# Kernel tuning notes

Hardware: AMD Instinct MI355X
Metric: run time of the kernel (lower is better)

## Reference

```python
import jax, jax.numpy as jnp
import numpy as np
import math

HEAD_DIM = 64
N_Q = 64
N_KV = 8
HIDDEN = 2880
SLIDING = 128
BASE = 150000.0
INIT_CTX = 4096
SCALE = 32.0
NTK_A = 1.0
NTK_B = 32.0
SEQ = 2048


def _rope_cos_sin(position_ids):
    # YaRN-scaled inverse frequencies (scaling_factor > 1 branch)
    freq = BASE ** (jnp.arange(0, HEAD_DIM, 2, dtype=jnp.float32) / HEAD_DIM)
    concentration = 0.1 * math.log(SCALE) + 1.0
    d_half = HEAD_DIM // 2
    low = d_half * math.log(INIT_CTX / (NTK_B * 2 * math.pi)) / math.log(BASE)
    high = d_half * math.log(INIT_CTX / (NTK_A * 2 * math.pi)) / math.log(BASE)
    interpolation = 1.0 / (SCALE * freq)
    extrapolation = 1.0 / freq
    ramp = (jnp.arange(d_half, dtype=jnp.float32) - low) / (high - low)
    mask = 1.0 - jnp.clip(ramp, 0.0, 1.0)
    inv_freq = interpolation * (1.0 - mask) + extrapolation * mask
    freqs = position_ids.astype(jnp.float32)[:, None] * inv_freq[None, :]  # [n, d/2]
    return jnp.cos(freqs) * concentration, jnp.sin(freqs) * concentration


def _apply_rope(x, cos, sin):
    # x: [n, h, d]; cos/sin: [n, d/2]
    cos = cos[:, None, :].astype(x.dtype)
    sin = sin[:, None, :].astype(x.dtype)
    x1, x2 = jnp.split(x, 2, axis=-1)
    return jnp.concatenate([x1 * cos - x2 * sin, x2 * cos + x1 * sin], axis=-1)


def setup_inputs() -> dict:
    key = jax.random.key(0)
    ks = jax.random.split(key, 6)
    qkv_dim = HEAD_DIM * (N_Q + 2 * N_KV)
    return {
        "hidden_states": jax.random.normal(ks[0], (SEQ, HIDDEN), dtype=jnp.float32),
        "qkv_w": jax.random.normal(ks[1], (qkv_dim, HIDDEN), dtype=jnp.float32) * 0.02,
        "qkv_b": jax.random.normal(ks[2], (qkv_dim,), dtype=jnp.float32) * 0.02,
        "o_w": jax.random.normal(ks[3], (HIDDEN, N_Q * HEAD_DIM), dtype=jnp.float32) * 0.02,
        "o_b": jax.random.normal(ks[4], (HIDDEN,), dtype=jnp.float32) * 0.02,
        "sinks": jax.random.normal(ks[5], (N_Q,), dtype=jnp.float32),
        "position_ids": jnp.arange(SEQ, dtype=jnp.int64 if jax.config.jax_enable_x64 else jnp.int32),
    }


def reference(hidden_states, qkv_w, qkv_b, o_w, o_b, sinks, position_ids):
    n = hidden_states.shape[0]
    scaling = HEAD_DIM ** (-0.5)

    # fused QKV projection + split
    qkv = hidden_states @ qkv_w.T + qkv_b  # [n, (nq+2*nkv)*d]
    q_sz, k_sz = N_Q * HEAD_DIM, N_KV * HEAD_DIM
    q = qkv[:, :q_sz].reshape(n, N_Q, HEAD_DIM)
    k = qkv[:, q_sz:q_sz + k_sz].reshape(n, N_KV, HEAD_DIM)
    v = qkv[:, q_sz + k_sz:].reshape(n, N_KV, HEAD_DIM)

    # RoPE (YaRN)
    cos, sin = _rope_cos_sin(position_ids)
    q = _apply_rope(q, cos, sin)
    k = _apply_rope(k, cos, sin)

    # GQA: repeat KV heads to match query heads
    groups = N_Q // N_KV
    k_full = jnp.repeat(k, groups, axis=1)  # [n, N_Q, d]
    v_full = jnp.repeat(v, groups, axis=1)

    scores = jnp.einsum('qhd,khd->hqk', q, k_full) * scaling  # [H, S, S]

    # sliding-window mask (distance > window -> -inf), as in source (no causal term)
    current_pos = position_ids.max()
    key_pos = current_pos - n + 1 + jnp.arange(n)
    dist = position_ids[:, None] - key_pos[None, :]
    win_mask = jnp.where(dist > SLIDING, -jnp.inf, 0.0).astype(scores.dtype)
    scores = scores + win_mask[None, :, :]

    # learned sink logit appended to softmax normalization
    sink = jnp.broadcast_to(sinks[:, None, None], (N_Q, n, 1)).astype(scores.dtype)
    logits = jnp.concatenate([scores, sink], axis=-1)  # [H, S, S+1]
    probs = jax.nn.softmax(logits, axis=-1)[..., :-1]   # drop sink column

    attn = jnp.einsum('hqk,khd->qhd', probs, v_full)    # [S, H, d]
    attn = attn.reshape(n, N_Q * HEAD_DIM)
    return attn @ o_w.T + o_b
```

## Files before the change

### kernel.cpp

```cpp
#include <hip/hip_runtime.h>
#include <hip/hip_bf16.h>
#include <stdint.h>

typedef __attribute__((ext_vector_type(4))) float f32x4;
typedef __attribute__((ext_vector_type(8))) short bf16x8;

#define SEQ 2048
#define HIDDEN 2880
#define NQ 64
#define NKV 8
#define HD 64
#define QKV_DIM 5120
#define Q_SZ 4096
#define K_SZ 512
#define OW_N 2880
#define OW_NPAD 2944
#define OW_K 4096

__device__ __forceinline__ unsigned short f2b_bits(float f) {
    unsigned int x = __float_as_uint(f);
    unsigned int r = (x + 0x7fffu + ((x >> 16) & 1u)) >> 16;
    return (unsigned short)r;
}
__device__ __forceinline__ float b2f(unsigned short u) {
    return __uint_as_float(((unsigned int)u) << 16);
}

__device__ __forceinline__ void llds16(const ushort* g, ushort* l) {
    __builtin_amdgcn_global_load_lds(
        (const __attribute__((address_space(1))) void*)g,
        (__attribute__((address_space(3))) void*)l, 16, 0, 0);
}

__global__ void convert_all(const float* __restrict__ hidden, const float* __restrict__ qkv_w,
                            const float* __restrict__ o_w, ushort* __restrict__ hs_bf,
                            ushort* __restrict__ wqkv_bf, ushort* __restrict__ wo_bf) {
    const int N1 = SEQ * HIDDEN / 4;
    const int N2 = N1 + QKV_DIM * HIDDEN / 4;
    const int N3 = N2 + OW_NPAD * OW_K / 4;
    int i = blockIdx.x * blockDim.x + threadIdx.x;
    int stride = gridDim.x * blockDim.x;
    for (; i < N3; i += stride) {
        const float* src;
        ushort* dst;
        int j;
        if (i < N1) {
            j = i; src = hidden; dst = hs_bf;
        } else if (i < N2) {
            j = i - N1; src = qkv_w; dst = wqkv_bf;
        } else {
            j = i - N2; src = o_w; dst = wo_bf;
            if ((j >> 10) >= OW_N) {
                reinterpret_cast<ushort4*>(dst)[j] = make_ushort4(0, 0, 0, 0);
                continue;
            }
        }
        float4 v = reinterpret_cast<const float4*>(src)[j];
        reinterpret_cast<ushort4*>(dst)[j] =
            make_ushort4(f2b_bits(v.x), f2b_bits(v.y), f2b_bits(v.z), f2b_bits(v.w));
    }
}

template<int OUT_BF16>
__global__ __launch_bounds__(256) void gemm_bt(
    const ushort* __restrict__ A, const ushort* __restrict__ B,
    const float* __restrict__ bias, void* __restrict__ Cout,
    int M, int N, int K, int Nreal, int ldC)
{
    __shared__ __align__(16) ushort As[128 * 64];
    __shared__ __align__(16) ushort Bs[128 * 64];
    const int tid = threadIdx.x;
    const int lane = tid & 63;
    const int w = tid >> 6;
    const int wr = w >> 1, wc = w & 1;

    const int nwg = gridDim.x;
    const int per = nwg >> 3;
    const int wgid = (blockIdx.x & 7) * per + (blockIdx.x >> 3);
    const int m0 = (wgid & 15) * 128;
    const int n0 = (wgid >> 4) * 128;

    f32x4 acc[4][4] = {};

    for (int k0 = 0; k0 < K; k0 += 64) {
        #pragma unroll
        for (int it = 0; it < 4; ++it) {
            int i = it * 256 + tid;
            int row = i >> 3;
            int col16 = (i ^ (row & 7)) & 7;
            const ushort* ga = A + (size_t)(m0 + row) * K + k0 + col16 * 8;
            ushort* la = As + (size_t)(it * 256 + (tid & ~63)) * 8;
            llds16(ga, la);
            const ushort* gb = B + (size_t)(n0 + row) * K + k0 + col16 * 8;
            ushort* lb = Bs + (size_t)(it * 256 + (tid & ~63)) * 8;
            llds16(gb, lb);
        }
        __syncthreads();
        #pragma unroll
        for (int kk = 0; kk < 2; ++kk) {
            bf16x8 a[4], b[4];
            #pragma unroll
            for (int mi = 0; mi < 4; ++mi) {
                int row = wr * 64 + mi * 16 + (lane & 15);
                int byte = row * 128 + kk * 64 + (lane >> 4) * 16;
                byte ^= (row & 7) << 4;
                a[mi] = *reinterpret_cast<const bf16x8*>(reinterpret_cast<const char*>(As) + byte);
            }
            #pragma unroll
            for (int ni = 0; ni < 4; ++ni) {
                int row = wc * 64 + ni * 16 + (lane & 15);
                int byte = row * 128 + kk * 64 + (lane >> 4) * 16;
                byte ^= (row & 7) << 4;
                b[ni] = *reinterpret_cast<const bf16x8*>(reinterpret_cast<const char*>(Bs) + byte);
            }
            #pragma unroll
            for (int mi = 0; mi < 4; ++mi)
                #pragma unroll
                for (int ni = 0; ni < 4; ++ni)
                    acc[mi][ni] = __builtin_amdgcn_mfma_f32_16x16x32_bf16(a[mi], b[ni], acc[mi][ni], 0, 0, 0);
        }
        __syncthreads();
    }

    #pragma unroll
    for (int mi = 0; mi < 4; ++mi) {
        int gr = m0 + wr * 64 + mi * 16 + (lane >> 4) * 4;
        #pragma unroll
        for (int ni = 0; ni < 4; ++ni) {
            int gc = n0 + wc * 64 + ni * 16 + (lane & 15);
            if (gc < Nreal) {
                float bv = bias[gc];
                #pragma unroll
                for (int r = 0; r < 4; ++r) {
                    float v = acc[mi][ni][r] + bv;
                    if (OUT_BF16)
                        ((ushort*)Cout)[(size_t)(gr + r) * ldC + gc] = f2b_bits(v);
                    else
                        ((float*)Cout)[(size_t)(gr + r) * ldC + gc] = v;
                }
            }
        }
    }
}

__global__ __launch_bounds__(256) void rope_kernel(
    const ushort* __restrict__ qkv, const int* __restrict__ pos,
    ushort* __restrict__ q_ro, ushort* __restrict__ k_ro)
{
    __shared__ float cosv[32], sinv[32];
    const int s = blockIdx.x;
    const int tid = threadIdx.x;
    if (tid < 32) {
        int j = tid;
        const float logbase = logf(150000.0f);
        float freq = expf((float)j * (logbase / 32.0f));
        float interp = 1.0f / (32.0f * freq);
        float extrap = 1.0f / freq;
        const float twopi = 6.283185307179586f;
        float low  = 32.0f * logf(4096.0f / (32.0f * twopi)) / logbase;
        float high = 32.0f * logf(4096.0f / (1.0f  * twopi)) / logbase;
        float ramp = ((float)j - low) / (high - low);
        float mask = 1.0f - fminf(fmaxf(ramp, 0.0f), 1.0f);
        float inv_freq = interp * (1.0f - mask) + extrap * mask;
        float ang = (float)pos[s] * inv_freq;
        const float conc = 0.1f * logf(32.0f) + 1.0f;
        cosv[j] = cosf(ang) * conc;
        sinv[j] = sinf(ang) * conc;
    }
    __syncthreads();
    const float qsc = 0.125f * 1.4426950408889634f;
    #pragma unroll
    for (int it = 0; it < 8; ++it) {
        int idx = it * 256 + tid;
        int h = idx >> 5, j = idx & 31;
        const ushort* src = qkv + (size_t)s * QKV_DIM + h * HD;
        float x1 = b2f(src[j]), x2 = b2f(src[j + 32]);
        float c = cosv[j], sn = sinv[j];
        ushort* dst = q_ro + ((size_t)h * SEQ + s) * HD;
        dst[j]      = f2b_bits((x1 * c - x2 * sn) * qsc);
        dst[j + 32] = f2b_bits((x2 * c + x1 * sn) * qsc);
    }
    {
        int h = tid >> 5, j = tid & 31;
        const ushort* src = qkv + (size_t)s * QKV_DIM + Q_SZ + h * HD;
        float x1 = b2f(src[j]), x2 = b2f(src[j + 32]);
        float c = cosv[j], sn = sinv[j];
        ushort* dst = k_ro + ((size_t)h * SEQ + s) * HD;
        dst[j]      = f2b_bits(x1 * c - x2 * sn);
        dst[j + 32] = f2b_bits(x2 * c + x1 * sn);
    }
}

__global__ __launch_bounds__(256) void vtrans_kernel(const ushort* __restrict__ qkv, ushort* __restrict__ vT) {
    __shared__ ushort t[64][65];
    const int kh = blockIdx.x >> 5;
    const int s0 = (blockIdx.x & 31) * 64;
    const int tid = threadIdx.x;
    #pragma unroll
    for (int it = 0; it < 16; ++it) {
        int e = it * 256 + tid;
        int sl = e >> 6, d = e & 63;
        t[d][sl] = qkv[(size_t)(s0 + sl) * QKV_DIM + Q_SZ + K_SZ + kh * HD + d];
    }
    __syncthreads();
    #pragma unroll
    for (int it = 0; it < 16; ++it) {
        int e = it * 256 + tid;
        int d = e >> 6, sl = e & 63;
        vT[((size_t)kh * HD + d) * SEQ + s0 + sl] = t[d][sl];
    }
}

__global__ __launch_bounds__(256, 4) void attn_kernel(
    const ushort* __restrict__ q_ro, const ushort* __restrict__ k_ro,
    const ushort* __restrict__ vT, const float* __restrict__ sinks,
    ushort* __restrict__ attn_out)
{
    __shared__ __align__(16) ushort Kb[2][4096];
    __shared__ __align__(16) ushort Vb[2][4096];
    __shared__ __align__(16) ushort Pl[4][1024];

    const int tid = threadIdx.x;
    const int lane = tid & 63;
    const int w = tid >> 6;
    const int l15 = lane & 15;
    const int l4 = lane >> 4;

    int wg = blockIdx.x;
    int wgid = (wg & 7) * 128 + (wg >> 3);
    const int kh = wgid >> 7;
    const int qh = (wgid >> 4) & 7;
    const int pp = wgid & 15;
    const int h = kh * 8 + qh;

    const float snk = sinks[h];
    char* pbase = (char*)&Pl[w][0];

    const short oneb = (short)0x3F80;
    const bf16x8 bones = {oneb, oneb, oneb, oneb, oneb, oneb, oneb, oneb};

    const int i0 = tid, i1 = 256 + tid;
    const int r0 = i0 >> 3, cs0 = (i0 ^ r0) & 7;
    const int r1 = i1 >> 3, cs1 = (i1 ^ r1) & 7;
    const ushort* gK0 = k_ro + (size_t)kh * (SEQ * 64) + r0 * 64 + cs0 * 8;
    const ushort* gK1 = k_ro + (size_t)kh * (SEQ * 64) + r1 * 64 + cs1 * 8;
    const ushort* gV0 = vT + ((size_t)kh * 64 + r0) * SEQ + cs0 * 8;
    const ushort* gV1 = vT + ((size_t)kh * 64 + r1) * SEQ + cs1 * 8;
    const int ld0 = (tid & ~63) * 8, ld1 = (256 + (tid & ~63)) * 8;

    const int swz = (l15 & 7) << 4;
    const int kvbase = l15 * 128 + ((l4 * 16) ^ swz);
    const int pwbase = l15 * 128 + ((l4 * 8) ^ swz);

    auto stage = [&](int bs, int k0) {
        llds16(gK0 + k0 * 64, &Kb[bs][ld0]);
        llds16(gK1 + k0 * 64, &Kb[bs][ld1]);
        llds16(gV0 + k0,      &Vb[bs][ld0]);
        llds16(gV1 + k0,      &Vb[bs][ld1]);
    };

    for (int sidx = 0; sidx < 2; ++sidx) {
        const int qt = sidx ? (31 - pp) : pp;
        const int q0 = qt * 64;
        const int qw = q0 + w * 16;

        bf16x8 aq[2];
        #pragma unroll
        for (int kc = 0; kc < 2; ++kc)
            aq[kc] = *reinterpret_cast<const bf16x8*>(
                q_ro + ((size_t)h * SEQ + qw + l15) * HD + kc * 32 + l4 * 8);

        f32x4 o[4] = {};
        f32x4 lacc = {0.f, 0.f, 0.f, 0.f};

        const int kt0 = (qt >= 2) ? (qt - 2) : 0;
        int cur = 0;

        stage(0, kt0 * 64);
        __syncthreads();

        for (int kt = kt0; kt < SEQ / 64; ++kt) {
            const int k0 = kt * 64;
            if (kt + 1 < SEQ / 64) stage(cur ^ 1, k0 + 64);

            f32x4 s[4];
            const f32x4 z = {0.f, 0.f, 0.f, 0.f};
            const char* kbp = (const char*)Kb[cur];
            __builtin_amdgcn_s_setprio(1);
            #pragma unroll
            for (int c = 0; c < 4; ++c) {
                bf16x8 bk0 = *reinterpret_cast<const bf16x8*>(kbp + c * 2048 + kvbase);
                s[c] = __builtin_amdgcn_mfma_f32_16x16x32_bf16(bk0, aq[0], z, 0, 0, 0);
                bf16x8 bk1 = *reinterpret_cast<const bf16x8*>(kbp + c * 2048 + (kvbase ^ 64));
                s[c] = __builtin_amdgcn_mfma_f32_16x16x32_bf16(bk1, aq[1], s[c], 0, 0, 0);
            }
            __builtin_amdgcn_s_setprio(0);

            if (k0 < qw - 113) {
                int thr = qw + l15 - 128 - k0;
                #pragma unroll
                for (int c = 0; c < 4; ++c)
                    #pragma unroll
                    for (int r = 0; r < 4; ++r)
                        if (c * 16 + l4 * 4 + r < thr) s[c][r] = -1e30f;
            }

            #pragma unroll
            for (int c = 0; c < 4; ++c) {
                float p0 = exp2f(s[c][0]), p1 = exp2f(s[c][1]);
                float p2 = exp2f(s[c][2]), p3 = exp2f(s[c][3]);
                unsigned int pk0, pk1;
                asm("v_cvt_pk_bf16_f32 %0, %1, %2" : "=v"(pk0) : "v"(p0), "v"(p1));
                asm("v_cvt_pk_bf16_f32 %0, %1, %2" : "=v"(pk1) : "v"(p2), "v"(p3));
                uint2 pv; pv.x = pk0; pv.y = pk1;
                *reinterpret_cast<uint2*>(pbase + (pwbase ^ (c * 32))) = pv;
            }

            const char* vbp = (const char*)Vb[cur];
            __builtin_amdgcn_s_setprio(1);
            #pragma unroll
            for (int kc = 0; kc < 2; ++kc) {
                bf16x8 pa = *reinterpret_cast<const bf16x8*>(pbase + (kvbase ^ (kc * 64)));
                lacc = __builtin_amdgcn_mfma_f32_16x16x32_bf16(pa, bones, lacc, 0, 0, 0);
                #pragma unroll
                for (int df = 0; df < 4; ++df) {
                    bf16x8 bv = *reinterpret_cast<const bf16x8*>(vbp + df * 2048 + (kvbase ^ (kc * 64)));
                    o[df] = __builtin_amdgcn_mfma_f32_16x16x32_bf16(pa, bv, o[df], 0, 0, 0);
                }
            }
            __builtin_amdgcn_s_setprio(0);

            __syncthreads();
            cur ^= 1;
        }

        {
            const float es = exp2f(snk * 1.4426950408889634f);
            float inv[4];
            #pragma unroll
            for (int r = 0; r < 4; ++r) inv[r] = 1.0f / (lacc[r] + es);
            #pragma unroll
            for (int df = 0; df < 4; ++df)
                #pragma unroll
                for (int r = 0; r < 4; ++r) {
                    int row = qw + l4 * 4 + r;
                    int col = df * 16 + l15;
                    attn_out[(size_t)row * Q_SZ + h * HD + col] = f2b_bits(o[df][r] * inv[r]);
                }
        }
    }
}

extern "C" void kernel_launch(void* const* d_in, const int* in_sizes, int n_in,
                              void* d_out, int out_size, void* d_ws, size_t ws_size,
                              hipStream_t stream) {
    const float* hidden = (const float*)d_in[0];
    const float* qkv_w  = (const float*)d_in[1];
    const float* qkv_b  = (const float*)d_in[2];
    const float* o_w    = (const float*)d_in[3];
    const float* o_b    = (const float*)d_in[4];
    const float* sinks  = (const float*)d_in[5];
    const int*   pos    = (const int*)d_in[6];
    float* out = (float*)d_out;

    char* ws = (char*)d_ws;
    size_t off = 0;
    auto alloc = [&](size_t bytes) {
        char* p = ws + off;
        off += (bytes + 255) & ~(size_t)255;
        return p;
    };
    ushort* hs_bf   = (ushort*)alloc((size_t)SEQ * HIDDEN * 2);
    ushort* wqkv_bf = (ushort*)alloc((size_t)QKV_DIM * HIDDEN * 2);
    ushort* qkv_bf  = (ushort*)alloc((size_t)SEQ * QKV_DIM * 2);
    ushort* q_ro    = (ushort*)alloc((size_t)NQ * SEQ * HD * 2);
    ushort* k_ro    = (ushort*)alloc((size_t)NKV * SEQ * HD * 2);
    ushort* vT      = (ushort*)alloc((size_t)NKV * HD * SEQ * 2);
    ushort* attn_bf = (ushort*)alloc((size_t)SEQ * Q_SZ * 2);
    ushort* wo_bf   = (ushort*)alloc((size_t)OW_NPAD * OW_K * 2);

    convert_all<<<2048, 256, 0, stream>>>(hidden, qkv_w, o_w, hs_bf, wqkv_bf, wo_bf);

    gemm_bt<1><<<(QKV_DIM / 128) * (SEQ / 128), 256, 0, stream>>>(
        hs_bf, wqkv_bf, qkv_b, qkv_bf, SEQ, QKV_DIM, HIDDEN, QKV_DIM, QKV_DIM);

    rope_kernel<<<SEQ, 256, 0, stream>>>(qkv_bf, pos, q_ro, k_ro);
    vtrans_kernel<<<NKV * 32, 256, 0, stream>>>(qkv_bf, vT);

    attn_kernel<<<1024, 256, 0, stream>>>(q_ro, k_ro, vT, sinks, attn_bf);

    gemm_bt<0><<<(OW_NPAD / 128) * (SEQ / 128), 256, 0, stream>>>(
        attn_bf, wo_bf, o_b, out, SEQ, OW_NPAD, OW_K, OW_N, OW_N);
}
```

Baseline: 272.7 us.

## Use 64x128 GEMM tiles and single-buffer V with split barrier in attention

The GEMMs move from 128x128 to 64x128 tiles, which doubles the workgroup count to fill the device's CUs better. Each wave now covers all 64 rows by 32 columns, so A-tile reuse per wave goes up and B reuse goes down. The attention kernel shrinks V staging to one buffer, loaded at the start of each tile and awaited with a vmcnt wait plus barrier before the PV MFMAs. This cuts LDS use so more blocks can run per CU, at the cost of exposing V load latency behind the QK compute.

```diff
diff --git a/kernel.cpp b/kernel.cpp
--- a/kernel.cpp
+++ b/kernel.cpp
@@ -62,61 +62,66 @@
 }
 
 template<int OUT_BF16>
-__global__ __launch_bounds__(256) void gemm_bt(
+__global__ __launch_bounds__(256) void gemm_bt64(
     const ushort* __restrict__ A, const ushort* __restrict__ B,
     const float* __restrict__ bias, void* __restrict__ Cout,
     int M, int N, int K, int Nreal, int ldC)
 {
-    __shared__ __align__(16) ushort As[128 * 64];
+    __shared__ __align__(16) ushort As[64 * 64];
     __shared__ __align__(16) ushort Bs[128 * 64];
     const int tid = threadIdx.x;
     const int lane = tid & 63;
     const int w = tid >> 6;
-    const int wr = w >> 1, wc = w & 1;
+    const int l15 = lane & 15;
+    const int l4 = lane >> 4;
 
     const int nwg = gridDim.x;
     const int per = nwg >> 3;
     const int wgid = (blockIdx.x & 7) * per + (blockIdx.x >> 3);
-    const int m0 = (wgid & 15) * 128;
-    const int n0 = (wgid >> 4) * 128;
-
-    f32x4 acc[4][4] = {};
+    const int m0 = (wgid & 31) * 64;
+    const int n0 = (wgid >> 5) * 128;
+
+    f32x4 acc[4][2] = {};
 
     for (int k0 = 0; k0 < K; k0 += 64) {
+        #pragma unroll
+        for (int it = 0; it < 2; ++it) {
+            int i = it * 256 + tid;
+            int row = i >> 3;
+            int col16 = (i ^ (row & 7)) & 7;
+            llds16(A + (size_t)(m0 + row) * K + k0 + col16 * 8,
+                   As + (size_t)(it * 256 + (tid & ~63)) * 8);
+        }
         #pragma unroll
         for (int it = 0; it < 4; ++it) {
             int i = it * 256 + tid;
             int row = i >> 3;
             int col16 = (i ^ (row & 7)) & 7;
-            const ushort* ga = A + (size_t)(m0 + row) * K + k0 + col16 * 8;
-            ushort* la = As + (size_t)(it * 256 + (tid & ~63)) * 8;
-            llds16(ga, la);
-            const ushort* gb = B + (size_t)(n0 + row) * K + k0 + col16 * 8;
-            ushort* lb = Bs + (size_t)(it * 256 + (tid & ~63)) * 8;
-            llds16(gb, lb);
+            llds16(B + (size_t)(n0 + row) * K + k0 + col16 * 8,
+                   Bs + (size_t)(it * 256 + (tid & ~63)) * 8);
         }
         __syncthreads();
         #pragma unroll
         for (int kk = 0; kk < 2; ++kk) {
-            bf16x8 a[4], b[4];
+            bf16x8 a[4], b[2];
             #pragma unroll
             for (int mi = 0; mi < 4; ++mi) {
-                int row = wr * 64 + mi * 16 + (lane & 15);
-                int byte = row * 128 + kk * 64 + (lane >> 4) * 16;
+                int row = mi * 16 + l15;
+                int byte = row * 128 + kk * 64 + l4 * 16;
                 byte ^= (row & 7) << 4;
                 a[mi] = *reinterpret_cast<const bf16x8*>(reinterpret_cast<const char*>(As) + byte);
             }
             #pragma unroll
-            for (int ni = 0; ni < 4; ++ni) {
-                int row = wc * 64 + ni * 16 + (lane & 15);
-                int byte = row * 128 + kk * 64 + (lane >> 4) * 16;
+            for (int ni = 0; ni < 2; ++ni) {
+                int row = w * 32 + ni * 16 + l15;
+                int byte = row * 128 + kk * 64 + l4 * 16;
                 byte ^= (row & 7) << 4;
                 b[ni] = *reinterpret_cast<const bf16x8*>(reinterpret_cast<const char*>(Bs) + byte);
             }
             #pragma unroll
             for (int mi = 0; mi < 4; ++mi)
                 #pragma unroll
-                for (int ni = 0; ni < 4; ++ni)
+                for (int ni = 0; ni < 2; ++ni)
                     acc[mi][ni] = __builtin_amdgcn_mfma_f32_16x16x32_bf16(a[mi], b[ni], acc[mi][ni], 0, 0, 0);
         }
         __syncthreads();
@@ -124,10 +129,10 @@
 
     #pragma unroll
     for (int mi = 0; mi < 4; ++mi) {
-        int gr = m0 + wr * 64 + mi * 16 + (lane >> 4) * 4;
+        int gr = m0 + mi * 16 + l4 * 4;
         #pragma unroll
-        for (int ni = 0; ni < 4; ++ni) {
-            int gc = n0 + wc * 64 + ni * 16 + (lane & 15);
+        for (int ni = 0; ni < 2; ++ni) {
+            int gc = n0 + w * 32 + ni * 16 + l15;
             if (gc < Nreal) {
                 float bv = bias[gc];
                 #pragma unroll
@@ -217,7 +222,7 @@
     ushort* __restrict__ attn_out)
 {
     __shared__ __align__(16) ushort Kb[2][4096];
-    __shared__ __align__(16) ushort Vb[2][4096];
+    __shared__ __align__(16) ushort Vb[4096];
     __shared__ __align__(16) ushort Pl[4][1024];
 
     const int tid = threadIdx.x;
@@ -252,11 +257,13 @@
     const int kvbase = l15 * 128 + ((l4 * 16) ^ swz);
     const int pwbase = l15 * 128 + ((l4 * 8) ^ swz);
 
-    auto stage = [&](int bs, int k0) {
+    auto stageK = [&](int bs, int k0) {
         llds16(gK0 + k0 * 64, &Kb[bs][ld0]);
         llds16(gK1 + k0 * 64, &Kb[bs][ld1]);
-        llds16(gV0 + k0,      &Vb[bs][ld0]);
-        llds16(gV1 + k0,      &Vb[bs][ld1]);
+    };
+    auto stageV = [&](int k0) {
+        llds16(gV0 + k0, &Vb[ld0]);
+        llds16(gV1 + k0, &Vb[ld1]);
     };
 
     for (int sidx = 0; sidx < 2; ++sidx) {
@@ -276,12 +283,13 @@
         const int kt0 = (qt >= 2) ? (qt - 2) : 0;
         int cur = 0;
 
-        stage(0, kt0 * 64);
+        stageK(0, kt0 * 64);
         __syncthreads();
 
-        for (int kt = kt0; kt < SEQ / 64; ++kt) {
+        auto tile_body = [&](int kt, bool pref) {
             const int k0 = kt * 64;
-            if (kt + 1 < SEQ / 64) stage(cur ^ 1, k0 + 64);
+            stageV(k0);
+            if (pref) stageK(cur ^ 1, k0 + 64);
 
             f32x4 s[4];
             const f32x4 z = {0.f, 0.f, 0.f, 0.f};
@@ -316,7 +324,10 @@
                 *reinterpret_cast<uint2*>(pbase + (pwbase ^ (c * 32))) = pv;
             }
 
-            const char* vbp = (const char*)Vb[cur];
+            if (pref) asm volatile("s_waitcnt vmcnt(2)\n\ts_barrier" ::: "memory");
+            else      asm volatile("s_waitcnt vmcnt(0)\n\ts_barrier" ::: "memory");
+
+            const char* vbp = (const char*)Vb;
             __builtin_amdgcn_s_setprio(1);
             #pragma unroll
             for (int kc = 0; kc < 2; ++kc) {
@@ -332,7 +343,10 @@
 
             __syncthreads();
             cur ^= 1;
-        }
+        };
+
+        for (int kt = kt0; kt < SEQ / 64 - 1; ++kt) tile_body(kt, true);
+        tile_body(SEQ / 64 - 1, false);
 
         {
             const float es = exp2f(snk * 1.4426950408889634f);
@@ -381,7 +395,7 @@
 
     convert_all<<<2048, 256, 0, stream>>>(hidden, qkv_w, o_w, hs_bf, wqkv_bf, wo_bf);
 
-    gemm_bt<1><<<(QKV_DIM / 128) * (SEQ / 128), 256, 0, stream>>>(
+    gemm_bt64<1><<<(QKV_DIM / 128) * (SEQ / 64), 256, 0, stream>>>(
         hs_bf, wqkv_bf, qkv_b, qkv_bf, SEQ, QKV_DIM, HIDDEN, QKV_DIM, QKV_DIM);
 
     rope_kernel<<<SEQ, 256, 0, stream>>>(qkv_bf, pos, q_ro, k_ro);
@@ -389,6 +403,6 @@
 
     attn_kernel<<<1024, 256, 0, stream>>>(q_ro, k_ro, vT, sinks, attn_bf);
 
-    gemm_bt<0><<<(OW_NPAD / 128) * (SEQ / 128), 256, 0, stream>>>(
+    gemm_bt64<0><<<(OW_NPAD / 128) * (SEQ / 64), 256, 0, stream>>>(
         attn_bf, wo_bf, o_b, out, SEQ, OW_NPAD, OW_K, OW_N, OW_N);
 }
```

Result: no change. 275.3 us (+0.9%).
